# Optimization experiments

Hardware: AMD Instinct MI355X
Metric: run time of the kernel (lower is better)

## Reference

```python
import jax, jax.numpy as jnp
import numpy as np

PH = 32          # prediction horizon (unroll steps)
HID = 512        # hidden_dim == latent_dim (output fed back as input)
OUT = 2          # output_dim
BS = 2048


def setup_inputs() -> dict:
    key = jax.random.key(0)
    ks = jax.random.split(key, 8)
    s = 1.0 / np.sqrt(HID)
    return {
        "hist": jax.random.normal(ks[0], (BS, 8, 2), dtype=jnp.float32),
        "z": jax.random.normal(ks[1], (BS, 1, HID), dtype=jnp.float32),
        # LSTMCell params (PyTorch layout: [4H, in], gate order i,f,g,o)
        "W_ih": jax.random.uniform(ks[2], (4 * HID, HID), jnp.float32, -s, s),
        "W_hh": jax.random.uniform(ks[3], (4 * HID, HID), jnp.float32, -s, s),
        "b_ih": jax.random.uniform(ks[4], (4 * HID,), jnp.float32, -s, s),
        "b_hh": jax.random.uniform(ks[5], (4 * HID,), jnp.float32, -s, s),
        # dense: hidden_dim -> output_dim
        "W_d": jax.random.uniform(ks[6], (OUT, HID), jnp.float32, -s, s),
        "b_d": jax.random.uniform(ks[7], (OUT,), jnp.float32, -s, s),
    }


def reference(hist, z, W_ih, W_hh, b_ih, b_hh, W_d, b_d):
    bs = z.shape[0]
    x0 = z.reshape(bs, -1)                       # [bs, H]
    h0 = jnp.zeros((bs, HID), dtype=z.dtype)
    c0 = jnp.zeros((bs, HID), dtype=z.dtype)

    def step(carry, _):
        x, h, c = carry
        gates = x @ W_ih.T + b_ih + h @ W_hh.T + b_hh   # [bs, 4H]
        i, f, g, o = jnp.split(gates, 4, axis=-1)
        c_new = jax.nn.sigmoid(f) * c + jax.nn.sigmoid(i) * jnp.tanh(g)
        h_new = jax.nn.sigmoid(o) * jnp.tanh(c_new)
        # output h is fed back as next input
        return (h_new, h_new, c_new), h_new

    _, hs = jax.lax.scan(step, (x0, h0, c0), None, length=PH)  # [PH, bs, H]
    out_all = jnp.swapaxes(hs, 0, 1)                           # [bs, PH, H]
    y = out_all @ W_d.T + b_d                                  # [bs, PH, OUT]
    return y
```

## Files before the change

### kernel.cpp

```cpp
#include <hip/hip_runtime.h>
#include <hip/hip_bf16.h>

#define BS_   2048
#define HID_  512
#define PH_   32
#define GRP_  16

typedef _Float16 half8 __attribute__((ext_vector_type(8)));
typedef float floatx4 __attribute__((ext_vector_type(4)));

__device__ __forceinline__ float sigf(float x) { return 1.f / (1.f + __expf(-x)); }
__device__ __forceinline__ float tanhfast(float x) {
    float e = __expf(2.f * x);
    return 1.f - 2.f / (e + 1.f);
}

__global__ __launch_bounds__(256) void prep_kernel(
    const float* __restrict__ Wih, const float* __restrict__ Whh,
    const float* __restrict__ bih, const float* __restrict__ bhh,
    const float* __restrict__ z,
    _Float16* __restrict__ wih16, _Float16* __restrict__ wsum16,
    _Float16* __restrict__ z16, float* __restrict__ bsum,
    int* __restrict__ cnt)
{
    int i = blockIdx.x * 256 + threadIdx.x;
    if (i < BS_ * HID_) z16[i] = (_Float16)z[i];
    if (i < 4 * HID_ * HID_) {
        float a = Wih[i];
        wih16[i]  = (_Float16)a;
        wsum16[i] = (_Float16)(a + Whh[i]);
    }
    if (i < 4 * HID_) bsum[i] = bih[i] + bhh[i];
    if (i < 512) cnt[i] = 0;
}

__device__ __forceinline__ void stage_weights(_Float16* Wl, const _Float16* Wg,
                                              int j, int tid)
{
#pragma unroll
    for (int rep = 0; rep < 16; ++rep) {
        int idx = rep * 512 + tid;
        int n  = idx >> 6;
        int kb = idx & 63;
        int g  = n >> 5, u = n & 31;
        const half8* src = (const half8*)(Wg + ((size_t)(g * HID_ + j * 32 + u)) * HID_ + kb * 8);
        int phys = (kb & 56) | ((kb & 7) ^ (n & 7));
        *(half8*)((char*)Wl + n * 1024 + phys * 16) = *src;
    }
}

__global__ __launch_bounds__(512) void lstm_persist(
    const _Float16* __restrict__ wih16, const _Float16* __restrict__ wsum16,
    const float* __restrict__ bsum, const _Float16* __restrict__ z16,
    _Float16* __restrict__ hs, int* __restrict__ cnt)
{
    __shared__ _Float16 Wl[128 * 512];

    const int tid  = threadIdx.x;
    const int ib   = blockIdx.x & 15;
    const int j    = blockIdx.x >> 4;
    const int lane = tid & 63;
    const int wv   = tid >> 6;
    const int ms   = wv & 3;
    const int hh   = wv >> 2;
    const int qw   = lane >> 4;
    const int ln   = lane & 15;
    const int hid  = j * 32 + hh * 16 + ln;

    stage_weights(Wl, wih16, j, tid);

    float bias[4];
#pragma unroll
    for (int g = 0; g < 4; ++g) bias[g] = bsum[g * HID_ + hid];

    float c[2][4];
#pragma unroll
    for (int mt = 0; mt < 2; ++mt)
#pragma unroll
        for (int r = 0; r < 4; ++r) c[mt][r] = 0.f;

    const char* Bl = (const char*)Wl;
    const int tE = (qw ^ (ln & 7)) * 16;
    const int rowB = hh * 16 + ln;

    __syncthreads();

    for (int t = 0; t < PH_; ++t) {
        const _Float16* xx = (t == 0) ? z16 : hs + (size_t)(t - 1) * BS_ * HID_;

        if (t >= 1) {
            if (tid == 0) {
                while (__hip_atomic_fetch_add(&cnt[ib * 32 + t - 1], 0,
                                              __ATOMIC_RELAXED,
                                              __HIP_MEMORY_SCOPE_AGENT) < GRP_) {
                    __builtin_amdgcn_s_sleep(1);
                }
            }
            __syncthreads();
        }

        floatx4 acc[2][4];
#pragma unroll
        for (int mt = 0; mt < 2; ++mt)
#pragma unroll
            for (int g = 0; g < 4; ++g)
                acc[mt][g] = (floatx4){bias[g], bias[g], bias[g], bias[g]};

        const _Float16* A0 = xx + (size_t)(ib * 128 + ms * 32 + ln) * HID_ + qw * 8;

        half8 a0r[4], a1r[4], bA[4], bB[4];
#pragma unroll
        for (int p = 0; p < 4; ++p) {
            a0r[p] = *(const half8*)(A0 + p * 32);
            a1r[p] = *(const half8*)(A0 + 16 * HID_ + p * 32);
        }
#pragma unroll
        for (int g = 0; g < 4; ++g)
            bA[g] = *(const half8*)(Bl + (g * 32 + rowB) * 1024 + tE);

#pragma unroll
        for (int kk = 0; kk < 16; ++kk) {
            half8 ca0 = a0r[kk & 3], ca1 = a1r[kk & 3];
            if (kk < 12) {
                a0r[kk & 3] = *(const half8*)(A0 + (kk + 4) * 32);
                a1r[kk & 3] = *(const half8*)(A0 + 16 * HID_ + (kk + 4) * 32);
            }
            half8* cb = (kk & 1) ? bB : bA;
            half8* nb = (kk & 1) ? bA : bB;
            if (kk < 15) {
                int k1 = kk + 1;
#pragma unroll
                for (int g = 0; g < 4; ++g) {
                    int off = (g * 32 + rowB) * 1024 + (k1 >> 1) * 128 + (tE ^ ((k1 & 1) << 6));
                    nb[g] = *(const half8*)(Bl + off);
                }
            }
#pragma unroll
            for (int g = 0; g < 4; ++g) {
                acc[0][g] = __builtin_amdgcn_mfma_f32_16x16x32_f16(ca0, cb[g], acc[0][g], 0, 0, 0);
                acc[1][g] = __builtin_amdgcn_mfma_f32_16x16x32_f16(ca1, cb[g], acc[1][g], 0, 0, 0);
            }
        }

        _Float16* hb = hs + (size_t)t * BS_ * HID_
                          + (size_t)(ib * 128 + ms * 32 + qw * 4) * HID_ + hid;
#pragma unroll
        for (int mt = 0; mt < 2; ++mt) {
#pragma unroll
            for (int r = 0; r < 4; ++r) {
                float gi = acc[mt][0][r];
                float gf = acc[mt][1][r];
                float gg = acc[mt][2][r];
                float go = acc[mt][3][r];
                float cn = sigf(gf) * c[mt][r] + sigf(gi) * tanhfast(gg);
                float hn = sigf(go) * tanhfast(cn);
                c[mt][r] = cn;
                _Float16 hf = (_Float16)hn;
                short hv;
                __builtin_memcpy(&hv, &hf, 2);
                __hip_atomic_store((short*)(hb + (size_t)(mt * 16 + r) * HID_), hv,
                                   __ATOMIC_RELAXED, __HIP_MEMORY_SCOPE_AGENT);
            }
        }

        __syncthreads();
        if (t == 0) {
            if (tid == 0)
                __hip_atomic_fetch_add(&cnt[ib * 32], 1,
                                       __ATOMIC_RELAXED, __HIP_MEMORY_SCOPE_AGENT);
            stage_weights(Wl, wsum16, j, tid);
            __syncthreads();
        } else if (t < PH_ - 1) {
            if (tid == 0)
                __hip_atomic_fetch_add(&cnt[ib * 32 + t], 1,
                                       __ATOMIC_RELAXED, __HIP_MEMORY_SCOPE_AGENT);
        }
    }
}

__global__ __launch_bounds__(256) void dense_kernel(
    const _Float16* __restrict__ hs, const float* __restrict__ Wd,
    const float* __restrict__ bd, float* __restrict__ y)
{
    int gw   = (blockIdx.x * 256 + threadIdx.x) >> 6;
    int lane = threadIdx.x & 63;
    int tt = gw & 31, b = gw >> 5;
    half8 h = *(const half8*)(hs + ((size_t)tt * BS_ + b) * HID_ + lane * 8);
    float s0 = 0.f, s1 = 0.f;
#pragma unroll
    for (int k = 0; k < 8; ++k) {
        float hv = (float)h[k];
        s0 += hv * Wd[lane * 8 + k];
        s1 += hv * Wd[HID_ + lane * 8 + k];
    }
#pragma unroll
    for (int m = 32; m >= 1; m >>= 1) {
        s0 += __shfl_xor(s0, m);
        s1 += __shfl_xor(s1, m);
    }
    if (lane == 0) {
        float* o = y + ((size_t)b * PH_ + tt) * 2;
        o[0] = s0 + bd[0];
        o[1] = s1 + bd[1];
    }
}

extern "C" void kernel_launch(void* const* d_in, const int* in_sizes, int n_in,
                              void* d_out, int out_size, void* d_ws, size_t ws_size,
                              hipStream_t stream)
{
    (void)in_sizes; (void)n_in; (void)out_size; (void)ws_size;
    const float* z   = (const float*)d_in[1];
    const float* Wih = (const float*)d_in[2];
    const float* Whh = (const float*)d_in[3];
    const float* bih = (const float*)d_in[4];
    const float* bhh = (const float*)d_in[5];
    const float* Wd  = (const float*)d_in[6];
    const float* bd  = (const float*)d_in[7];
    float* y = (float*)d_out;

    char* ws = (char*)d_ws;
    _Float16* hs     = (_Float16*)ws;
    _Float16* z16    = (_Float16*)(ws + (size_t)67108864);
    _Float16* wih16  = (_Float16*)(ws + (size_t)69206016);
    _Float16* wsum16 = (_Float16*)(ws + (size_t)71303168);
    float*    bsum   = (float*)   (ws + (size_t)73400320);
    int*      cnt    = (int*)     (ws + (size_t)73408512);

    prep_kernel<<<4096, 256, 0, stream>>>(Wih, Whh, bih, bhh, z,
                                          wih16, wsum16, z16, bsum, cnt);

    {
        const void* k = (const void*)lstm_persist;
        void* args[] = {(void*)&wih16, (void*)&wsum16, (void*)&bsum,
                        (void*)&z16, (void*)&hs, (void*)&cnt};
        hipLaunchCooperativeKernel(k, dim3(256), dim3(512), args, 0, stream);
    }

    dense_kernel<<<16384, 256, 0, stream>>>(hs, Wd, bd, y);
}
```

Measured before the change: 425.4 us.

## Use plain stores when batch group is on one XCC; batch dense kernel rows

Each block of the persistent LSTM records its XCC ID in a per-group handshake word and waits until all 16 blocks in the group have arrived. If the whole group sits on a single XCC, it writes h with plain stores instead of agent-scope atomic stores, which avoids the cross-die coherence cost. The dense output kernel now caches W_d in shared memory and registers, and each wave handles 8 rows, so it launches 8x fewer blocks. The handshake adds an extra grid-wide wait at startup, and the plain-store path relies on same-XCC L2 coherence.

```diff
diff --git a/kernel.cpp b/kernel.cpp
--- a/kernel.cpp
+++ b/kernel.cpp
@@ -69,6 +69,21 @@
 
     stage_weights(Wl, wih16, j, tid);
 
+    if (tid == 0) {
+        unsigned xcc = 0;
+        asm volatile("s_getreg_b32 %0, hwreg(HW_REG_XCC_ID)" : "=s"(xcc));
+        int bit = 1 << (8 + (int)(xcc & 15));
+        __hip_atomic_fetch_or(&cnt[ib * 32 + 31], bit,
+                              __ATOMIC_RELAXED, __HIP_MEMORY_SCOPE_AGENT);
+        __hip_atomic_fetch_add(&cnt[ib * 32 + 31], 1,
+                               __ATOMIC_RELAXED, __HIP_MEMORY_SCOPE_AGENT);
+        while ((__hip_atomic_fetch_add(&cnt[ib * 32 + 31], 0,
+                                       __ATOMIC_RELAXED,
+                                       __HIP_MEMORY_SCOPE_AGENT) & 0xff) < GRP_) {
+            __builtin_amdgcn_s_sleep(1);
+        }
+    }
+
     float bias[4];
 #pragma unroll
     for (int g = 0; g < 4; ++g) bias[g] = bsum[g * HID_ + hid];
@@ -84,6 +99,10 @@
     const int rowB = hh * 16 + ln;
 
     __syncthreads();
+
+    const int hsk = __hip_atomic_load(&cnt[ib * 32 + 31], __ATOMIC_RELAXED,
+                                      __HIP_MEMORY_SCOPE_AGENT);
+    const bool fastp = __popc(((unsigned)hsk) >> 8) == 1;
 
     for (int t = 0; t < PH_; ++t) {
         const _Float16* xx = (t == 0) ? z16 : hs + (size_t)(t - 1) * BS_ * HID_;
@@ -144,6 +163,7 @@
 
         _Float16* hb = hs + (size_t)t * BS_ * HID_
                           + (size_t)(ib * 128 + ms * 32 + qw * 4) * HID_ + hid;
+        short hvv[2][4];
 #pragma unroll
         for (int mt = 0; mt < 2; ++mt) {
 #pragma unroll
@@ -156,11 +176,23 @@
                 float hn = sigf(go) * tanhfast(cn);
                 c[mt][r] = cn;
                 _Float16 hf = (_Float16)hn;
-                short hv;
-                __builtin_memcpy(&hv, &hf, 2);
-                __hip_atomic_store((short*)(hb + (size_t)(mt * 16 + r) * HID_), hv,
-                                   __ATOMIC_RELAXED, __HIP_MEMORY_SCOPE_AGENT);
-            }
+                __builtin_memcpy(&hvv[mt][r], &hf, 2);
+            }
+        }
+        if (fastp) {
+#pragma unroll
+            for (int mt = 0; mt < 2; ++mt)
+#pragma unroll
+                for (int r = 0; r < 4; ++r)
+                    *(short*)(hb + (size_t)(mt * 16 + r) * HID_) = hvv[mt][r];
+        } else {
+#pragma unroll
+            for (int mt = 0; mt < 2; ++mt)
+#pragma unroll
+                for (int r = 0; r < 4; ++r)
+                    __hip_atomic_store((short*)(hb + (size_t)(mt * 16 + r) * HID_),
+                                       hvv[mt][r],
+                                       __ATOMIC_RELAXED, __HIP_MEMORY_SCOPE_AGENT);
         }
 
         __syncthreads();
@@ -182,26 +214,45 @@
     const _Float16* __restrict__ hs, const float* __restrict__ Wd,
     const float* __restrict__ bd, float* __restrict__ y)
 {
-    int gw   = (blockIdx.x * 256 + threadIdx.x) >> 6;
-    int lane = threadIdx.x & 63;
-    int tt = gw & 31, b = gw >> 5;
-    half8 h = *(const half8*)(hs + ((size_t)tt * BS_ + b) * HID_ + lane * 8);
-    float s0 = 0.f, s1 = 0.f;
+    __shared__ float4 WdL4[256];
+    const int tid = threadIdx.x;
+    WdL4[tid] = ((const float4*)Wd)[tid];
+    __syncthreads();
+    const float* WdL = (const float*)WdL4;
+
+    const int lane = tid & 63;
+    const int wv   = tid >> 6;
+    float wd0[8], wd1[8];
 #pragma unroll
     for (int k = 0; k < 8; ++k) {
-        float hv = (float)h[k];
-        s0 += hv * Wd[lane * 8 + k];
-        s1 += hv * Wd[HID_ + lane * 8 + k];
-    }
-#pragma unroll
-    for (int m = 32; m >= 1; m >>= 1) {
-        s0 += __shfl_xor(s0, m);
-        s1 += __shfl_xor(s1, m);
-    }
-    if (lane == 0) {
-        float* o = y + ((size_t)b * PH_ + tt) * 2;
-        o[0] = s0 + bd[0];
-        o[1] = s1 + bd[1];
+        wd0[k] = WdL[lane * 8 + k];
+        wd1[k] = WdL[HID_ + lane * 8 + k];
+    }
+    const float b0 = bd[0], b1 = bd[1];
+
+    const int base = (blockIdx.x * 4 + wv) * 8;
+#pragma unroll
+    for (int i = 0; i < 8; ++i) {
+        const int r  = base + i;
+        const int tt = r & 31, b = r >> 5;
+        half8 h = *(const half8*)(hs + ((size_t)tt * BS_ + b) * HID_ + lane * 8);
+        float s0 = 0.f, s1 = 0.f;
+#pragma unroll
+        for (int k = 0; k < 8; ++k) {
+            float hv = (float)h[k];
+            s0 += hv * wd0[k];
+            s1 += hv * wd1[k];
+        }
+#pragma unroll
+        for (int m = 32; m >= 1; m >>= 1) {
+            s0 += __shfl_xor(s0, m);
+            s1 += __shfl_xor(s1, m);
+        }
+        if (lane == 0) {
+            float* o = y + ((size_t)b * PH_ + tt) * 2;
+            o[0] = s0 + b0;
+            o[1] = s1 + b1;
+        }
     }
 }
 
@@ -237,5 +288,5 @@
         hipLaunchCooperativeKernel(k, dim3(256), dim3(512), args, 0, stream);
     }
 
-    dense_kernel<<<16384, 256, 0, stream>>>(hs, Wd, bd, y);
-}
+    dense_kernel<<<2048, 256, 0, stream>>>(hs, Wd, bd, y);
+}
```

Result: no change. 417.9 us (-1.7%).

## Fuse prep, LSTM recurrence and dense projection into one cooperative kernel

Applied to the files above, without the earlier changes.

Merges the fp16 conversion prep kernel and the dense output kernel into the persistent cooperative LSTM kernel, using grid-wide syncs between phases. The dense phase now has each wave process 32 rows with the dense weights cached in registers via LDS. This removes two kernel launches and their launch gaps. The cost is two grid barriers and a dense phase limited to 256 blocks instead of 16384, which may reduce how well that phase hides memory latency.

```diff
diff --git a/kernel.cpp b/kernel.cpp
--- a/kernel.cpp
+++ b/kernel.cpp
@@ -1,5 +1,8 @@
 #include <hip/hip_runtime.h>
 #include <hip/hip_bf16.h>
+#include <hip/hip_cooperative_groups.h>
+
+namespace cg = cooperative_groups;
 
 #define BS_   2048
 #define HID_  512
@@ -15,23 +18,13 @@
     return 1.f - 2.f / (e + 1.f);
 }
 
-__global__ __launch_bounds__(256) void prep_kernel(
-    const float* __restrict__ Wih, const float* __restrict__ Whh,
-    const float* __restrict__ bih, const float* __restrict__ bhh,
-    const float* __restrict__ z,
-    _Float16* __restrict__ wih16, _Float16* __restrict__ wsum16,
-    _Float16* __restrict__ z16, float* __restrict__ bsum,
-    int* __restrict__ cnt)
-{
-    int i = blockIdx.x * 256 + threadIdx.x;
-    if (i < BS_ * HID_) z16[i] = (_Float16)z[i];
-    if (i < 4 * HID_ * HID_) {
-        float a = Wih[i];
-        wih16[i]  = (_Float16)a;
-        wsum16[i] = (_Float16)(a + Whh[i]);
-    }
-    if (i < 4 * HID_) bsum[i] = bih[i] + bhh[i];
-    if (i < 512) cnt[i] = 0;
+__device__ __forceinline__ void st2h(_Float16* p, float x, float y) {
+    _Float16 h0 = (_Float16)x, h1 = (_Float16)y;
+    unsigned short u0, u1;
+    __builtin_memcpy(&u0, &h0, 2);
+    __builtin_memcpy(&u1, &h1, 2);
+    unsigned u = (unsigned)u0 | ((unsigned)u1 << 16);
+    __hip_atomic_store((unsigned*)p, u, __ATOMIC_RELAXED, __HIP_MEMORY_SCOPE_AGENT);
 }
 
 __device__ __forceinline__ void stage_weights(_Float16* Wl, const _Float16* Wg,
@@ -49,10 +42,15 @@
     }
 }
 
-__global__ __launch_bounds__(512) void lstm_persist(
-    const _Float16* __restrict__ wih16, const _Float16* __restrict__ wsum16,
-    const float* __restrict__ bsum, const _Float16* __restrict__ z16,
-    _Float16* __restrict__ hs, int* __restrict__ cnt)
+__global__ __launch_bounds__(512) void lstm_mega(
+    const float* __restrict__ Wih, const float* __restrict__ Whh,
+    const float* __restrict__ bih, const float* __restrict__ bhh,
+    const float* __restrict__ z,   const float* __restrict__ Wd,
+    const float* __restrict__ bd,
+    _Float16* __restrict__ wih16, _Float16* __restrict__ wsum16,
+    float* __restrict__ bsum, _Float16* __restrict__ z16,
+    _Float16* __restrict__ hs, int* __restrict__ cnt,
+    float* __restrict__ y)
 {
     __shared__ _Float16 Wl[128 * 512];
 
@@ -66,6 +64,37 @@
     const int qw   = lane >> 4;
     const int ln   = lane & 15;
     const int hid  = j * 32 + hh * 16 + ln;
+
+    {
+        const int gtid = blockIdx.x * 512 + tid;
+        const int base = gtid * 8;
+        float4 a0 = *(const float4*)(Wih + base);
+        float4 a1 = *(const float4*)(Wih + base + 4);
+        float4 b0 = *(const float4*)(Whh + base);
+        float4 b1 = *(const float4*)(Whh + base + 4);
+        st2h(wih16 + base,     a0.x, a0.y);
+        st2h(wih16 + base + 2, a0.z, a0.w);
+        st2h(wih16 + base + 4, a1.x, a1.y);
+        st2h(wih16 + base + 6, a1.z, a1.w);
+        st2h(wsum16 + base,     a0.x + b0.x, a0.y + b0.y);
+        st2h(wsum16 + base + 2, a0.z + b0.z, a0.w + b0.w);
+        st2h(wsum16 + base + 4, a1.x + b1.x, a1.y + b1.y);
+        st2h(wsum16 + base + 6, a1.z + b1.z, a1.w + b1.w);
+        float4 z0 = *(const float4*)(z + base);
+        float4 z1 = *(const float4*)(z + base + 4);
+        st2h(z16 + base,     z0.x, z0.y);
+        st2h(z16 + base + 2, z0.z, z0.w);
+        st2h(z16 + base + 4, z1.x, z1.y);
+        st2h(z16 + base + 6, z1.z, z1.w);
+        if (gtid < 4 * HID_)
+            __hip_atomic_store(bsum + gtid, bih[gtid] + bhh[gtid],
+                               __ATOMIC_RELAXED, __HIP_MEMORY_SCOPE_AGENT);
+        if (gtid < 512)
+            __hip_atomic_store(cnt + gtid, 0,
+                               __ATOMIC_RELAXED, __HIP_MEMORY_SCOPE_AGENT);
+        asm volatile("s_waitcnt vmcnt(0)" ::: "memory");
+    }
+    cg::this_grid().sync();
 
     stage_weights(Wl, wih16, j, tid);
 
@@ -176,32 +205,44 @@
                                        __ATOMIC_RELAXED, __HIP_MEMORY_SCOPE_AGENT);
         }
     }
-}
-
-__global__ __launch_bounds__(256) void dense_kernel(
-    const _Float16* __restrict__ hs, const float* __restrict__ Wd,
-    const float* __restrict__ bd, float* __restrict__ y)
-{
-    int gw   = (blockIdx.x * 256 + threadIdx.x) >> 6;
-    int lane = threadIdx.x & 63;
-    int tt = gw & 31, b = gw >> 5;
-    half8 h = *(const half8*)(hs + ((size_t)tt * BS_ + b) * HID_ + lane * 8);
-    float s0 = 0.f, s1 = 0.f;
+
+    cg::this_grid().sync();
+
+    float* WdL = (float*)Wl;
+    if (tid < 256) ((float4*)WdL)[tid] = ((const float4*)Wd)[tid];
+    __syncthreads();
+
+    float wd0[8], wd1[8];
 #pragma unroll
     for (int k = 0; k < 8; ++k) {
-        float hv = (float)h[k];
-        s0 += hv * Wd[lane * 8 + k];
-        s1 += hv * Wd[HID_ + lane * 8 + k];
-    }
-#pragma unroll
-    for (int m = 32; m >= 1; m >>= 1) {
-        s0 += __shfl_xor(s0, m);
-        s1 += __shfl_xor(s1, m);
-    }
-    if (lane == 0) {
-        float* o = y + ((size_t)b * PH_ + tt) * 2;
-        o[0] = s0 + bd[0];
-        o[1] = s1 + bd[1];
+        wd0[k] = WdL[lane * 8 + k];
+        wd1[k] = WdL[HID_ + lane * 8 + k];
+    }
+    const float b0 = bd[0], b1 = bd[1];
+
+    const int base = (blockIdx.x * 8 + wv) * 32;
+#pragma unroll 8
+    for (int i = 0; i < 32; ++i) {
+        const int r  = base + i;
+        const int tt = r & 31, b = r >> 5;
+        half8 h = *(const half8*)(hs + ((size_t)tt * BS_ + b) * HID_ + lane * 8);
+        float s0 = 0.f, s1 = 0.f;
+#pragma unroll
+        for (int k = 0; k < 8; ++k) {
+            float hv = (float)h[k];
+            s0 += hv * wd0[k];
+            s1 += hv * wd1[k];
+        }
+#pragma unroll
+        for (int m = 32; m >= 1; m >>= 1) {
+            s0 += __shfl_xor(s0, m);
+            s1 += __shfl_xor(s1, m);
+        }
+        if (lane == 0) {
+            float* o = y + ((size_t)b * PH_ + tt) * 2;
+            o[0] = s0 + b0;
+            o[1] = s1 + b1;
+        }
     }
 }
 
@@ -227,15 +268,10 @@
     float*    bsum   = (float*)   (ws + (size_t)73400320);
     int*      cnt    = (int*)     (ws + (size_t)73408512);
 
-    prep_kernel<<<4096, 256, 0, stream>>>(Wih, Whh, bih, bhh, z,
-                                          wih16, wsum16, z16, bsum, cnt);
-
-    {
-        const void* k = (const void*)lstm_persist;
-        void* args[] = {(void*)&wih16, (void*)&wsum16, (void*)&bsum,
-                        (void*)&z16, (void*)&hs, (void*)&cnt};
-        hipLaunchCooperativeKernel(k, dim3(256), dim3(512), args, 0, stream);
-    }
-
-    dense_kernel<<<16384, 256, 0, stream>>>(hs, Wd, bd, y);
-}
+    const void* k = (const void*)lstm_mega;
+    void* args[] = {(void*)&Wih, (void*)&Whh, (void*)&bih, (void*)&bhh,
+                    (void*)&z,   (void*)&Wd,  (void*)&bd,
+                    (void*)&wih16, (void*)&wsum16, (void*)&bsum,
+                    (void*)&z16, (void*)&hs, (void*)&cnt, (void*)&y};
+    hipLaunchCooperativeKernel(k, dim3(256), dim3(512), args, 0, stream);
+}
```

New measurement: 474.9 us. 11.6% more time.
